# Kernel tuning notes

Measured on AMD Instinct MI355X. Metric: run time of the kernel, lower is better.

## Reference

```python
import jax, jax.numpy as jnp
import numpy as np

B, S, F, H = 4, 8192, 1024, 16
D = F // H  # k_dim = 64
EPS = 1e-6


def setup_inputs() -> dict:
    rng = jax.random.key(0)
    ks = jax.random.split(rng, 6)
    # xavier-normal-ish scale for square (F, F) kernels
    w_std = float(np.sqrt(2.0 / (F + F)))
    return {
        "query": jax.random.normal(ks[0], (B, S, F), jnp.float32),
        "key": jax.random.normal(ks[1], (B, S, F), jnp.float32),
        "value": jax.random.normal(ks[2], (B, S, F), jnp.float32),
        "Wq": jax.random.normal(ks[3], (F, F), jnp.float32) * w_std,
        "Wk": jax.random.normal(ks[4], (F, F), jnp.float32) * w_std,
        "Wv": jax.random.normal(ks[5], (F, F), jnp.float32) * w_std,
        # per-head LayerNorm params for K and V (galerkin branch): (H, D)
        "ln_k_scale": jnp.ones((H, D), jnp.float32),
        "ln_k_bias": jnp.zeros((H, D), jnp.float32),
        "ln_v_scale": jnp.ones((H, D), jnp.float32),
        "ln_v_bias": jnp.zeros((H, D), jnp.float32),
    }


def _per_head_layernorm(x, scale, bias):
    # x: (B, H, N, D); scale/bias: (H, D) -> broadcast per head
    mu = jnp.mean(x, axis=-1, keepdims=True)
    var = jnp.var(x, axis=-1, keepdims=True)
    xn = (x - mu) * jax.lax.rsqrt(var + EPS)
    return xn * scale[None, :, None, :] + bias[None, :, None, :]


def reference(query, key, value, Wq, Wk, Wv, ln_k_scale, ln_k_bias, ln_v_scale, ln_v_bias):
    # QKV projections (no bias), then the module's raw contiguous reshape
    # (B, S, F) -> (B, H, S, D)  [NOT a head transpose -- faithful to source]
    q = jnp.matmul(query, Wq).reshape(B, H, -1, D)
    k = jnp.matmul(key, Wk).reshape(B, H, -1, D)
    v = jnp.matmul(value, Wv).reshape(B, H, -1, D)
    # galerkin: per-head LayerNorm on K and V only
    k = _per_head_layernorm(k, ln_k_scale, ln_k_bias)
    v = _per_head_layernorm(v, ln_v_scale, ln_v_bias)
    # linear (galerkin) attention: p_attn = K^T V / seq_len; out = Q p_attn
    seq_len = v.shape[-2]
    p_attn = jnp.einsum('bhnd,bhne->bhde', k, v) / seq_len  # (B, H, D, D)
    x = jnp.einsum('bhnd,bhde->bhne', q, p_attn)            # (B, H, N, D)
    att_output = x.reshape(B, -1, H * D)                    # (B, S, F)
    return (att_output, p_attn)
```

## Files before the change

### kernel.cpp

```cpp
#include <hip/hip_runtime.h>
#include <hip/hip_bf16.h>
#include <stdint.h>

#define DEVI __device__ __forceinline__

typedef __attribute__((ext_vector_type(8))) short bf16x8;
typedef __attribute__((ext_vector_type(4))) float f32x4;

static constexpr int Bb = 4, Ss = 8192, Ff = 1024, Hh = 16, Dd = 64;
static constexpr int Mm = Bb * Ss;
static constexpr int Kk = Ff;
static constexpr int PROJ_ELEMS = Mm * Ff;
static constexpr int NGROUP = PROJ_ELEMS / 64;

DEVI ushort f2bf(float f) {
  uint32_t u = __builtin_bit_cast(uint32_t, f);
  u += 0x7fffu + ((u >> 16) & 1u);
  return (ushort)(u >> 16);
}
DEVI float bf2f(ushort u) { return __builtin_bit_cast(float, (uint32_t)u << 16); }

DEVI uint32_t pack2(float a, float b) {
  return (uint32_t)f2bf(a) | ((uint32_t)f2bf(b) << 16);
}

DEVI void async16(void* lds, const void* g) {
  __builtin_amdgcn_global_load_lds((const __attribute__((address_space(1))) void*)g,
                                   (__attribute__((address_space(3))) void*)lds,
                                   16, 0, 0);
}

__global__ __launch_bounds__(256) void wt_kernel(const float* __restrict__ Wq,
                                                 const float* __restrict__ Wk,
                                                 const float* __restrict__ Wv,
                                                 ushort* __restrict__ wt) {
  __shared__ float tile[64][65];
  int b = blockIdx.x;
  const int w = b >> 8; b &= 255;
  const int kt = b >> 4, nt = b & 15;
  const float* Wsrc = (w == 0) ? Wq : ((w == 1) ? Wk : Wv);
  ushort* dst = wt + (size_t)w * 1024 * 1024;
  const int t = threadIdx.x;
  const int r = t >> 6, c = t & 63;
#pragma unroll
  for (int i = 0; i < 16; i++) {
    const int kk = kt * 64 + r + i * 4;
    tile[r + i * 4][c] = Wsrc[(size_t)kk * 1024 + nt * 64 + c];
  }
  __syncthreads();
#pragma unroll
  for (int i = 0; i < 16; i++) {
    const int nn = nt * 64 + r + i * 4;
    dst[(size_t)nn * 1024 + kt * 64 + c] = f2bf(tile[c][r + i * 4]);
  }
}

__global__ __launch_bounds__(256, 3) void gemm_qkv_kernel(
    const float* __restrict__ Aq, const float* __restrict__ Ak,
    const float* __restrict__ Av, const ushort* __restrict__ Wt,
    ushort* __restrict__ Cout) {
  __shared__ __align__(16) ushort As[128][64];
  __shared__ __align__(16) ushort Bs[128][64];

  const int bx = blockIdx.x;
  const int proj = bx >> 11;
  const int t2 = bx & 2047;
  const int mt = t2 >> 3;
  const int nt = t2 & 7;
  const float* A = (proj == 0) ? Aq : ((proj == 1) ? Ak : Av);
  const ushort* Bw = Wt + (size_t)proj * 1024 * 1024;
  ushort* C = Cout + (size_t)proj * PROJ_ELEMS;
  const int m0 = mt * 128, n0 = nt * 128;
  const int tid = threadIdx.x;
  const int lane = tid & 63;
  const int wave = tid >> 6;
  const int wy = wave >> 1, wx = wave & 1;

  const int ar = tid >> 3;
  const int ac = (tid & 7) * 8;
  const float* Abase = A + (size_t)m0 * Kk;

  const f32x4 fzero = {0.0f, 0.0f, 0.0f, 0.0f};
  f32x4 acc[4][4];
#pragma unroll
  for (int i = 0; i < 4; i++)
#pragma unroll
    for (int j = 0; j < 4; j++) acc[i][j] = fzero;

  for (int k0 = 0; k0 < Kk; k0 += 64) {
#pragma unroll
    for (int j = 0; j < 4; j++) {
      const int seg = wave * 4 + j;
      const int brow = seg * 8 + (lane >> 3);
      const int bcol = (lane & 7) * 8;
      async16(&Bs[seg * 8][0], Bw + (size_t)(n0 + brow) * Kk + k0 + bcol);
    }
#pragma unroll
    for (int i = 0; i < 4; i++) {
      const int row = ar + i * 32;
      const float* src = Abase + (size_t)row * Kk + k0 + ac;
      const float4 f0 = *(const float4*)src;
      const float4 f1 = *(const float4*)(src + 4);
      uint4 v;
      v.x = pack2(f0.x, f0.y);
      v.y = pack2(f0.z, f0.w);
      v.z = pack2(f1.x, f1.y);
      v.w = pack2(f1.z, f1.w);
      *(uint4*)&As[row][ac] = v;
    }
    __syncthreads();
#pragma unroll
    for (int ks = 0; ks < 2; ks++) {
      bf16x8 af[4], bv[4];
#pragma unroll
      for (int i = 0; i < 4; i++)
        af[i] = *(const bf16x8*)&As[wy * 64 + i * 16 + (lane & 15)][ks * 32 + (lane >> 4) * 8];
#pragma unroll
      for (int j = 0; j < 4; j++)
        bv[j] = *(const bf16x8*)&Bs[wx * 64 + j * 16 + (lane & 15)][ks * 32 + (lane >> 4) * 8];
#pragma unroll
      for (int i = 0; i < 4; i++)
#pragma unroll
        for (int j = 0; j < 4; j++)
          acc[i][j] = __builtin_amdgcn_mfma_f32_16x16x32_bf16(af[i], bv[j], acc[i][j], 0, 0, 0);
    }
    __syncthreads();
  }
#pragma unroll
  for (int i = 0; i < 4; i++) {
    const int rbase = m0 + wy * 64 + i * 16 + (lane >> 4) * 4;
#pragma unroll
    for (int j = 0; j < 4; j++) {
      const int col = n0 + wx * 64 + j * 16 + (lane & 15);
#pragma unroll
      for (int r = 0; r < 4; r++)
        C[(size_t)(rbase + r) * 1024 + col] = f2bf(acc[i][j][r]);
    }
  }
}

__global__ __launch_bounds__(256) void ln_kernel(
    ushort* __restrict__ kp, ushort* __restrict__ vp,
    const float* __restrict__ ksc, const float* __restrict__ kbi,
    const float* __restrict__ vsc, const float* __restrict__ vbi) {
  const int lane = threadIdx.x & 63;
  const int gwave = (blockIdx.x * 256 + threadIdx.x) >> 6;
  const int nw = (gridDim.x * 256) >> 6;
  const int sub = lane >> 3;
  const int off = (lane & 7) * 8;
  const int npass = NGROUP / 8;
  for (int p = gwave; p < npass; p += nw) {
    const size_t g = (size_t)p * 8 + sub;
    const int h = (int)((g >> 13) & 15);
    const size_t base = g * 64 + off;
#pragma unroll
    for (int which = 0; which < 2; which++) {
      ushort* ptr = which ? vp : kp;
      const float* sc = which ? vsc : ksc;
      const float* bi = which ? vbi : kbi;
      const uint4 raw = *(const uint4*)(ptr + base);
      const uint32_t* rw = (const uint32_t*)&raw;
      float x[8];
#pragma unroll
      for (int j = 0; j < 4; j++) {
        x[2 * j] = bf2f((ushort)(rw[j] & 0xffffu));
        x[2 * j + 1] = bf2f((ushort)(rw[j] >> 16));
      }
      float s = 0.f, sq = 0.f;
#pragma unroll
      for (int j = 0; j < 8; j++) { s += x[j]; sq += x[j] * x[j]; }
      s += __shfl_xor(s, 1); s += __shfl_xor(s, 2); s += __shfl_xor(s, 4);
      sq += __shfl_xor(sq, 1); sq += __shfl_xor(sq, 2); sq += __shfl_xor(sq, 4);
      const float mean = s * (1.0f / 64.0f);
      const float var = sq * (1.0f / 64.0f) - mean * mean;
      const float rs = rsqrtf(var + 1e-6f);
      uint4 outv;
      uint32_t* ow = (uint32_t*)&outv;
#pragma unroll
      for (int j = 0; j < 4; j++) {
        const int d0 = off + 2 * j;
        const float y0 = (x[2 * j] - mean) * rs * sc[h * 64 + d0] + bi[h * 64 + d0];
        const float y1 = (x[2 * j + 1] - mean) * rs * sc[h * 64 + d0 + 1] + bi[h * 64 + d0 + 1];
        ow[j] = pack2(y0, y1);
      }
      *(uint4*)(ptr + base) = outv;
    }
  }
}

__global__ __launch_bounds__(256) void pattn_kernel(const ushort* __restrict__ kp,
                                                    const ushort* __restrict__ vp,
                                                    float* __restrict__ praw) {
  __shared__ __align__(16) ushort kT[64][72];
  __shared__ __align__(16) ushort vT[64][72];
  const int bh = blockIdx.x >> 3;
  const int nc = blockIdx.x & 7;
  const ushort* kb = kp + ((size_t)bh << 19) + (size_t)nc * 65536;
  const ushort* vb = vp + ((size_t)bh << 19) + (size_t)nc * 65536;
  const int tid = threadIdx.x;
  const int lane = tid & 63;
  const int wave = tid >> 6;
  const int d0 = wave * 16;
  const f32x4 fzero = {0.0f, 0.0f, 0.0f, 0.0f};
  f32x4 acc[4];
#pragma unroll
  for (int e = 0; e < 4; e++) acc[e] = fzero;

  for (int c = 0; c < 16; c++) {
    const ushort* kc = kb + c * 4096;
    const ushort* vc = vb + c * 4096;
    const uint4 ka = *(const uint4*)(kc + (size_t)lane * 64 + d0);
    const uint4 ka2 = *(const uint4*)(kc + (size_t)lane * 64 + d0 + 8);
    const uint4 va = *(const uint4*)(vc + (size_t)lane * 64 + d0);
    const uint4 va2 = *(const uint4*)(vc + (size_t)lane * 64 + d0 + 8);
    __syncthreads();
    const uint32_t* kw = (const uint32_t*)&ka;
    const uint32_t* kw2 = (const uint32_t*)&ka2;
    const uint32_t* vw = (const uint32_t*)&va;
    const uint32_t* vw2 = (const uint32_t*)&va2;
#pragma unroll
    for (int j = 0; j < 4; j++) {
      kT[d0 + 2 * j][lane] = (ushort)(kw[j] & 0xffffu);
      kT[d0 + 2 * j + 1][lane] = (ushort)(kw[j] >> 16);
      kT[d0 + 8 + 2 * j][lane] = (ushort)(kw2[j] & 0xffffu);
      kT[d0 + 8 + 2 * j + 1][lane] = (ushort)(kw2[j] >> 16);
      vT[d0 + 2 * j][lane] = (ushort)(vw[j] & 0xffffu);
      vT[d0 + 2 * j + 1][lane] = (ushort)(vw[j] >> 16);
      vT[d0 + 8 + 2 * j][lane] = (ushort)(vw2[j] & 0xffffu);
      vT[d0 + 8 + 2 * j + 1][lane] = (ushort)(vw2[j] >> 16);
    }
    __syncthreads();
#pragma unroll
    for (int ks = 0; ks < 2; ks++) {
      const bf16x8 af = *(const bf16x8*)&kT[wave * 16 + (lane & 15)][ks * 32 + (lane >> 4) * 8];
#pragma unroll
      for (int e = 0; e < 4; e++) {
        const bf16x8 bv = *(const bf16x8*)&vT[e * 16 + (lane & 15)][ks * 32 + (lane >> 4) * 8];
        acc[e] = __builtin_amdgcn_mfma_f32_16x16x32_bf16(af, bv, acc[e], 0, 0, 0);
      }
    }
  }
#pragma unroll
  for (int e = 0; e < 4; e++)
#pragma unroll
    for (int r = 0; r < 4; r++) {
      const int drow = wave * 16 + (lane >> 4) * 4 + r;
      const int ecol = e * 16 + (lane & 15);
      atomicAdd(&praw[(size_t)bh * 4096 + drow * 64 + ecol], acc[e][r]);
    }
}

__global__ __launch_bounds__(256) void scalep_kernel(const float* __restrict__ praw,
                                                     float* __restrict__ pout) {
  const int i = blockIdx.x * 256 + threadIdx.x;
  pout[i] = praw[i] * (1.0f / 8192.0f);
}

__global__ __launch_bounds__(256) void outgemm_kernel(const ushort* __restrict__ qp,
                                                      const float* __restrict__ praw,
                                                      float* __restrict__ xout) {
  __shared__ __align__(16) ushort pT[64][72];
  const int bh = blockIdx.x >> 4;
  const int mc = blockIdx.x & 15;
  const ushort* qb = qp + ((size_t)bh << 19) + (size_t)mc * 512 * 64;
  float* ob = xout + ((size_t)bh << 19) + (size_t)mc * 512 * 64;
  const float* pb = praw + (size_t)bh * 4096;
  const int tid = threadIdx.x;
  const int lane = tid & 63;
  const int wave = tid >> 6;
  for (int i = tid; i < 4096; i += 256) {
    const int d = i >> 6, e = i & 63;
    pT[e][d] = f2bf(pb[i] * (1.0f / 8192.0f));
  }
  __syncthreads();
  bf16x8 bv[4][2];
#pragma unroll
  for (int e = 0; e < 4; e++)
#pragma unroll
    for (int ks = 0; ks < 2; ks++)
      bv[e][ks] = *(const bf16x8*)&pT[e * 16 + (lane & 15)][ks * 32 + (lane >> 4) * 8];
  const f32x4 fzero = {0.0f, 0.0f, 0.0f, 0.0f};
  for (int it = 0; it < 8; it++) {
    const int rbase = it * 64 + wave * 16;
    const ushort* qrow = qb + (size_t)rbase * 64;
    const bf16x8 a0 = *(const bf16x8*)(qrow + (size_t)(lane & 15) * 64 + (lane >> 4) * 8);
    const bf16x8 a1 = *(const bf16x8*)(qrow + (size_t)(lane & 15) * 64 + (lane >> 4) * 8 + 32);
    f32x4 acc[4];
#pragma unroll
    for (int e = 0; e < 4; e++) acc[e] = fzero;
#pragma unroll
    for (int e = 0; e < 4; e++) {
      acc[e] = __builtin_amdgcn_mfma_f32_16x16x32_bf16(a0, bv[e][0], acc[e], 0, 0, 0);
      acc[e] = __builtin_amdgcn_mfma_f32_16x16x32_bf16(a1, bv[e][1], acc[e], 0, 0, 0);
    }
#pragma unroll
    for (int e = 0; e < 4; e++)
#pragma unroll
      for (int r = 0; r < 4; r++)
        ob[(size_t)(rbase + (lane >> 4) * 4 + r) * 64 + e * 16 + (lane & 15)] = acc[e][r];
  }
}

extern "C" void kernel_launch(void* const* d_in, const int* in_sizes, int n_in,
                              void* d_out, int out_size, void* d_ws, size_t ws_size,
                              hipStream_t stream) {
  const float* q_in = (const float*)d_in[0];
  const float* k_in = (const float*)d_in[1];
  const float* v_in = (const float*)d_in[2];
  const float* Wq = (const float*)d_in[3];
  const float* Wk = (const float*)d_in[4];
  const float* Wv = (const float*)d_in[5];
  const float* ksc = (const float*)d_in[6];
  const float* kbi = (const float*)d_in[7];
  const float* vsc = (const float*)d_in[8];
  const float* vbi = (const float*)d_in[9];

  ushort* q_proj = (ushort*)d_ws;
  ushort* k_proj = q_proj + (size_t)PROJ_ELEMS;
  ushort* v_proj = k_proj + (size_t)PROJ_ELEMS;
  ushort* wtb = v_proj + (size_t)PROJ_ELEMS;
  float* praw = (float*)(wtb + (size_t)3 * 1024 * 1024);

  float* att = (float*)d_out;
  float* pout = att + (size_t)PROJ_ELEMS;

  wt_kernel<<<768, 256, 0, stream>>>(Wq, Wk, Wv, wtb);
  gemm_qkv_kernel<<<6144, 256, 0, stream>>>(q_in, k_in, v_in, wtb, q_proj);
  ln_kernel<<<1024, 256, 0, stream>>>(k_proj, v_proj, ksc, kbi, vsc, vbi);
  (void)hipMemsetAsync(praw, 0, (size_t)Bb * Hh * 64 * 64 * sizeof(float), stream);
  pattn_kernel<<<512, 256, 0, stream>>>(k_proj, v_proj, praw);
  scalep_kernel<<<1024, 256, 0, stream>>>(praw, pout);
  outgemm_kernel<<<1024, 256, 0, stream>>>(q_proj, praw, att);
}
```

Baseline: 897.1 us.

## Fuse per-head LayerNorm into QKV GEMM epilogue and widen pattn grid

Computes the K/V per-head LayerNorm directly on GEMM accumulators using 16-lane shuffles, removing the separate LN kernel and its extra read/write pass over K and V. Also remaps block indices so consecutive blocks spread across N tiles and projections, and splits pattn into 4x more blocks with shorter sequence chunks for more parallelism. The trade-off is more atomic accumulation into praw and extra epilogue work in the GEMM.

```diff
diff --git a/kernel.cpp b/kernel.cpp
--- a/kernel.cpp
+++ b/kernel.cpp
@@ -11,7 +11,6 @@
 static constexpr int Mm = Bb * Ss;
 static constexpr int Kk = Ff;
 static constexpr int PROJ_ELEMS = Mm * Ff;
-static constexpr int NGROUP = PROJ_ELEMS / 64;
 
 DEVI ushort f2bf(float f) {
   uint32_t u = __builtin_bit_cast(uint32_t, f);
@@ -58,11 +57,14 @@
 __global__ __launch_bounds__(256, 3) void gemm_qkv_kernel(
     const float* __restrict__ Aq, const float* __restrict__ Ak,
     const float* __restrict__ Av, const ushort* __restrict__ Wt,
-    ushort* __restrict__ Cout) {
+    ushort* __restrict__ Cout,
+    const float* __restrict__ ksc, const float* __restrict__ kbi,
+    const float* __restrict__ vsc, const float* __restrict__ vbi) {
   __shared__ __align__(16) ushort As[128][64];
   __shared__ __align__(16) ushort Bs[128][64];
 
-  const int bx = blockIdx.x;
+  const int bx0 = blockIdx.x;
+  const int bx = (bx0 & 7) * 768 + (bx0 >> 3);
   const int proj = bx >> 11;
   const int t2 = bx & 2047;
   const int mt = t2 >> 3;
@@ -126,64 +128,56 @@
     }
     __syncthreads();
   }
-#pragma unroll
-  for (int i = 0; i < 4; i++) {
-    const int rbase = m0 + wy * 64 + i * 16 + (lane >> 4) * 4;
+
+  if (proj == 0) {
+#pragma unroll
+    for (int i = 0; i < 4; i++) {
+      const int rbase = m0 + wy * 64 + i * 16 + (lane >> 4) * 4;
+#pragma unroll
+      for (int j = 0; j < 4; j++) {
+        const int col = n0 + wx * 64 + j * 16 + (lane & 15);
+#pragma unroll
+        for (int r = 0; r < 4; r++)
+          C[(size_t)(rbase + r) * 1024 + col] = f2bf(acc[i][j][r]);
+      }
+    }
+  } else {
+    const float* sc = (proj == 1) ? ksc : vsc;
+    const float* bi = (proj == 1) ? kbi : vbi;
+    const int h = (m0 >> 9) & 15;
+    float scv[4], biv[4];
 #pragma unroll
     for (int j = 0; j < 4; j++) {
-      const int col = n0 + wx * 64 + j * 16 + (lane & 15);
-#pragma unroll
-      for (int r = 0; r < 4; r++)
-        C[(size_t)(rbase + r) * 1024 + col] = f2bf(acc[i][j][r]);
-    }
-  }
-}
-
-__global__ __launch_bounds__(256) void ln_kernel(
-    ushort* __restrict__ kp, ushort* __restrict__ vp,
-    const float* __restrict__ ksc, const float* __restrict__ kbi,
-    const float* __restrict__ vsc, const float* __restrict__ vbi) {
-  const int lane = threadIdx.x & 63;
-  const int gwave = (blockIdx.x * 256 + threadIdx.x) >> 6;
-  const int nw = (gridDim.x * 256) >> 6;
-  const int sub = lane >> 3;
-  const int off = (lane & 7) * 8;
-  const int npass = NGROUP / 8;
-  for (int p = gwave; p < npass; p += nw) {
-    const size_t g = (size_t)p * 8 + sub;
-    const int h = (int)((g >> 13) & 15);
-    const size_t base = g * 64 + off;
-#pragma unroll
-    for (int which = 0; which < 2; which++) {
-      ushort* ptr = which ? vp : kp;
-      const float* sc = which ? vsc : ksc;
-      const float* bi = which ? vbi : kbi;
-      const uint4 raw = *(const uint4*)(ptr + base);
-      const uint32_t* rw = (const uint32_t*)&raw;
-      float x[8];
-#pragma unroll
-      for (int j = 0; j < 4; j++) {
-        x[2 * j] = bf2f((ushort)(rw[j] & 0xffffu));
-        x[2 * j + 1] = bf2f((ushort)(rw[j] >> 16));
+      const int d = j * 16 + (lane & 15);
+      scv[j] = sc[h * 64 + d];
+      biv[j] = bi[h * 64 + d];
+    }
+#pragma unroll
+    for (int i = 0; i < 4; i++) {
+      const int rbase = m0 + wy * 64 + i * 16 + (lane >> 4) * 4;
+#pragma unroll
+      for (int r = 0; r < 4; r++) {
+        float s = 0.f, sq = 0.f;
+#pragma unroll
+        for (int j = 0; j < 4; j++) {
+          const float x = acc[i][j][r];
+          s += x;
+          sq += x * x;
+        }
+        s += __shfl_xor(s, 1); s += __shfl_xor(s, 2);
+        s += __shfl_xor(s, 4); s += __shfl_xor(s, 8);
+        sq += __shfl_xor(sq, 1); sq += __shfl_xor(sq, 2);
+        sq += __shfl_xor(sq, 4); sq += __shfl_xor(sq, 8);
+        const float mean = s * (1.0f / 64.0f);
+        const float var = sq * (1.0f / 64.0f) - mean * mean;
+        const float rs = rsqrtf(var + 1e-6f);
+#pragma unroll
+        for (int j = 0; j < 4; j++) {
+          const int col = n0 + wx * 64 + j * 16 + (lane & 15);
+          C[(size_t)(rbase + r) * 1024 + col] =
+              f2bf((acc[i][j][r] - mean) * rs * scv[j] + biv[j]);
+        }
       }
-      float s = 0.f, sq = 0.f;
-#pragma unroll
-      for (int j = 0; j < 8; j++) { s += x[j]; sq += x[j] * x[j]; }
-      s += __shfl_xor(s, 1); s += __shfl_xor(s, 2); s += __shfl_xor(s, 4);
-      sq += __shfl_xor(sq, 1); sq += __shfl_xor(sq, 2); sq += __shfl_xor(sq, 4);
-      const float mean = s * (1.0f / 64.0f);
-      const float var = sq * (1.0f / 64.0f) - mean * mean;
-      const float rs = rsqrtf(var + 1e-6f);
-      uint4 outv;
-      uint32_t* ow = (uint32_t*)&outv;
-#pragma unroll
-      for (int j = 0; j < 4; j++) {
-        const int d0 = off + 2 * j;
-        const float y0 = (x[2 * j] - mean) * rs * sc[h * 64 + d0] + bi[h * 64 + d0];
-        const float y1 = (x[2 * j + 1] - mean) * rs * sc[h * 64 + d0 + 1] + bi[h * 64 + d0 + 1];
-        ow[j] = pack2(y0, y1);
-      }
-      *(uint4*)(ptr + base) = outv;
     }
   }
 }
@@ -193,10 +187,10 @@
                                                     float* __restrict__ praw) {
   __shared__ __align__(16) ushort kT[64][72];
   __shared__ __align__(16) ushort vT[64][72];
-  const int bh = blockIdx.x >> 3;
-  const int nc = blockIdx.x & 7;
-  const ushort* kb = kp + ((size_t)bh << 19) + (size_t)nc * 65536;
-  const ushort* vb = vp + ((size_t)bh << 19) + (size_t)nc * 65536;
+  const int bh = blockIdx.x >> 5;
+  const int nc = blockIdx.x & 31;
+  const ushort* kb = kp + ((size_t)bh << 19) + (size_t)nc * 16384;
+  const ushort* vb = vp + ((size_t)bh << 19) + (size_t)nc * 16384;
   const int tid = threadIdx.x;
   const int lane = tid & 63;
   const int wave = tid >> 6;
@@ -206,7 +200,7 @@
 #pragma unroll
   for (int e = 0; e < 4; e++) acc[e] = fzero;
 
-  for (int c = 0; c < 16; c++) {
+  for (int c = 0; c < 4; c++) {
     const ushort* kc = kb + c * 4096;
     const ushort* vc = vb + c * 4096;
     const uint4 ka = *(const uint4*)(kc + (size_t)lane * 64 + d0);
@@ -325,10 +319,10 @@
   float* pout = att + (size_t)PROJ_ELEMS;
 
   wt_kernel<<<768, 256, 0, stream>>>(Wq, Wk, Wv, wtb);
-  gemm_qkv_kernel<<<6144, 256, 0, stream>>>(q_in, k_in, v_in, wtb, q_proj);
-  ln_kernel<<<1024, 256, 0, stream>>>(k_proj, v_proj, ksc, kbi, vsc, vbi);
+  gemm_qkv_kernel<<<6144, 256, 0, stream>>>(q_in, k_in, v_in, wtb, q_proj,
+                                            ksc, kbi, vsc, vbi);
   (void)hipMemsetAsync(praw, 0, (size_t)Bb * Hh * 64 * 64 * sizeof(float), stream);
-  pattn_kernel<<<512, 256, 0, stream>>>(k_proj, v_proj, praw);
+  pattn_kernel<<<2048, 256, 0, stream>>>(k_proj, v_proj, praw);
   scalep_kernel<<<1024, 256, 0, stream>>>(praw, pout);
   outgemm_kernel<<<1024, 256, 0, stream>>>(q_proj, praw, att);
 }
```

After: 816.3 us. 9.0% less time.
